# Kernel optimization log

Hardware: AMD Instinct MI355X
Metric: run time of the kernel (lower is better)

## Reference

```python
import jax, jax.numpy as jnp
import numpy as np
import itertools

R = 32  # voxel resolution
B, CIN, COUT, N, SD = 4, 32, 64, 32768, 256


def group_norm(x, gamma, beta, eps=1e-5):
    # torch GroupNorm with g = min(8, C) adjusted for divisibility
    C = x.shape[1]
    g = min(8, C)
    while g > 1 and C % g:
        g -= 1
    b = x.shape[0]
    xs = x.reshape(b, g, C // g, -1)
    mu = xs.mean(axis=(2, 3), keepdims=True)
    var = xs.var(axis=(2, 3), keepdims=True)
    xn = ((xs - mu) / jnp.sqrt(var + eps)).reshape(x.shape)
    shp = (1, C) + (1,) * (x.ndim - 2)
    return xn * gamma.reshape(shp) + beta.reshape(shp)


def conv1x1(w, x):  # w: (O, C), x: (B, C, N)
    return jnp.einsum('oc,bcn->bon', w, x)


def conv3d(x, w):  # x: (B,C,D,H,W), w: (O,I,3,3,3), padding 1
    return jax.lax.conv_general_dilated(x, w, (1, 1, 1), 'SAME',
                                        dimension_numbers=('NCDHW', 'OIDHW', 'NCDHW'))


def normalize_coords(coords):  # (B,N,3) -> [0, R-1]
    vmin = coords.min(axis=1, keepdims=True)
    vmax = coords.max(axis=1, keepdims=True)
    return (coords - vmin) / jnp.maximum(vmax - vmin, 1e-8) * (R - 1)


def voxelize(feats_bcn, norm):  # average voxelization via scatter-add
    b, C, n = feats_bcn.shape
    idx = jnp.clip(jnp.round(norm), 0, R - 1).astype(jnp.int32)  # (B,N,3)
    flat = (idx[..., 0] * R + idx[..., 1]) * R + idx[..., 2]  # (B,N)
    f_bnc = feats_bcn.transpose(0, 2, 1)
    seg = jax.vmap(lambda f, i: jax.ops.segment_sum(f, i, num_segments=R ** 3))(f_bnc, flat)
    cnt = jax.vmap(lambda i: jax.ops.segment_sum(jnp.ones((n,), feats_bcn.dtype), i, num_segments=R ** 3))(flat)
    vox = seg / jnp.maximum(cnt, 1.0)[..., None]  # (B, R^3, C)
    return vox.transpose(0, 2, 1).reshape(b, C, R, R, R)


def devoxelize(vox, norm):  # trilinear interpolation gather
    b, C = vox.shape[:2]
    n = norm.shape[1]
    f = jnp.clip(norm, 0.0, R - 1)
    x0 = jnp.floor(f)
    fr = f - x0
    x0i = x0.astype(jnp.int32)
    idxs, wts = [], []
    for d in itertools.product((0, 1), repeat=3):
        dv = jnp.array(d, jnp.int32)
        ci = jnp.minimum(x0i + dv, R - 1)  # (B,N,3)
        w = jnp.prod(jnp.where(jnp.array(d, bool), fr, 1.0 - fr), axis=-1)  # (B,N)
        idxs.append((ci[..., 0] * R + ci[..., 1]) * R + ci[..., 2])
        wts.append(w)
    idx8 = jnp.stack(idxs, axis=-1)  # (B,N,8)
    w8 = jnp.stack(wts, axis=-1)  # (B,N,8)
    vf = vox.reshape(b, C, R ** 3)
    g = jnp.take_along_axis(vf, idx8.reshape(b, 1, n * 8), axis=2).reshape(b, C, n, 8)
    return jnp.einsum('bcnk,bnk->bcn', g, w8)


def setup_inputs() -> dict:
    key = jax.random.key(0)
    ks = jax.random.split(key, 12)
    s = 0.05
    return {
        'feats': jax.random.normal(ks[0], (B, CIN, N), jnp.float32),
        'coords': jax.random.uniform(ks[1], (B, N, 3), jnp.float32),
        'style': jax.random.normal(ks[2], (B, SD), jnp.float32),
        'w_pin': jax.random.normal(ks[3], (COUT, CIN), jnp.float32) * s,
        'g_pin': jnp.ones((COUT,), jnp.float32), 'b_pin': jnp.zeros((COUT,), jnp.float32),
        'w_v1': jax.random.normal(ks[4], (COUT, COUT, 3, 3, 3), jnp.float32) * s,
        'g_v1': jnp.ones((COUT,), jnp.float32), 'b_v1': jnp.zeros((COUT,), jnp.float32),
        'w_v2': jax.random.normal(ks[5], (COUT, COUT, 3, 3, 3), jnp.float32) * s,
        'g_v2': jnp.ones((COUT,), jnp.float32), 'b_v2': jnp.zeros((COUT,), jnp.float32),
        'w_fuse': jax.random.normal(ks[6], (COUT, COUT), jnp.float32) * s,
        'g_f': jnp.ones((COUT,), jnp.float32), 'b_f': jnp.zeros((COUT,), jnp.float32),
        'w_skip': jax.random.normal(ks[7], (COUT, CIN), jnp.float32) * s,
        'w_as': jax.random.normal(ks[8], (COUT, SD), jnp.float32) * s,
        'b_as': jnp.zeros((COUT,), jnp.float32),
        'w_ab': jax.random.normal(ks[9], (COUT, SD), jnp.float32) * s,
        'b_ab': jnp.zeros((COUT,), jnp.float32),
    }


def reference(feats, coords, style, w_pin, g_pin, b_pin, w_v1, g_v1, b_v1,
              w_v2, g_v2, b_v2, w_fuse, g_f, b_f, w_skip, w_as, b_as, w_ab, b_ab):
    silu = jax.nn.silu
    x_in = silu(group_norm(conv1x1(w_pin, feats), g_pin, b_pin))  # point_in
    norm = normalize_coords(coords)
    vox = voxelize(x_in, norm)
    vox = silu(group_norm(conv3d(vox, w_v1), g_v1, b_v1))
    vox = silu(group_norm(conv3d(vox, w_v2), g_v2, b_v2))
    devox = devoxelize(vox, norm)
    out = silu(group_norm(conv1x1(w_fuse, devox), g_f, b_f))  # fuse
    out = out + conv1x1(w_skip, feats)  # skip (c_in != c_out)
    s = (style @ w_as.T + b_as)[..., None]  # AdaIN scale (B, C, 1)
    bb = (style @ w_ab.T + b_ab)[..., None]
    return out * (1.0 + s) + bb
```

## Files before the change

### kernel.cpp

```cpp
#include <hip/hip_runtime.h>
#include <hip/hip_bf16.h>
#include <math.h>

#define RR   32
#define RB   4
#define CIN  32
#define CO   64
#define NP   32768
#define SD   256
#define NVOX (RR*RR*RR)
#define GRP  8
#define CPG  8
#define GN_CNT 262144.0f
#define PR   34
#define PSLICE (PR*PR*CO)
#define PROW   (PR*CO)
#define PVOL   ((size_t)PR*PR*PR*CO)
#define WSL   73728

typedef __attribute__((ext_vector_type(8))) short short8;
typedef __attribute__((ext_vector_type(4))) float f32x4;
typedef __attribute__((ext_vector_type(16))) float f32x16;

__device__ inline float silu_f(float x){ return x / (1.f + __expf(-x)); }
__device__ inline float bf2f(ushort u){ uint v = ((uint)u)<<16; return *(float*)&v; }
__device__ inline ushort f2bf(float x){ __hip_bfloat16 h = __float2bfloat16(x); return *(ushort*)&h; }

__global__ void k_wpack(const float* __restrict__ w, short* __restrict__ wp){
    int i = blockIdx.x*256 + threadIdx.x;
    if (i >= 27*4*2*64) return;
    int l  = i & 63;
    int nt = (i>>6) & 1;
    int kc = (i>>7) & 3;
    int t  = i>>9;
    int oc = nt*32 + (l&31);
    int cib = kc*16 + (l>>5)*8;
    ushort out[8];
    #pragma unroll
    for (int j=0;j<8;j++) out[j] = f2bf(w[((oc*CO + cib + j))*27 + t]);
    *(uint4*)(wp + (size_t)i*8) = *(uint4*)out;
}

__global__ void k_adain(const float* __restrict__ style, const float* __restrict__ w_as,
                        const float* __restrict__ b_as, const float* __restrict__ w_ab,
                        const float* __restrict__ b_ab, float* __restrict__ sout,
                        float* __restrict__ bout){
    int t = threadIdx.x;
    int b = t >> 6, o = t & 63;
    const float* st = style + b*SD;
    float accs = b_as[o], accb = b_ab[o];
    for (int k=0;k<SD;k++){ float sv = st[k]; accs += sv*w_as[o*SD+k]; accb += sv*w_ab[o*SD+k]; }
    sout[t]=accs; bout[t]=accb;
}

__global__ void k_minmax(const float* __restrict__ coords, float* __restrict__ vmm){
    int b = blockIdx.x; int t = threadIdx.x;
    float mn[3]={1e30f,1e30f,1e30f}, mx[3]={-1e30f,-1e30f,-1e30f};
    const float* cp = coords + (size_t)b*NP*3;
    for (int n=t;n<NP;n+=256){
        #pragma unroll
        for(int d=0;d<3;d++){ float v = cp[n*3+d]; mn[d]=fminf(mn[d],v); mx[d]=fmaxf(mx[d],v);}
    }
    __shared__ float smn[256][3], smx[256][3];
    #pragma unroll
    for(int d=0;d<3;d++){ smn[t][d]=mn[d]; smx[t][d]=mx[d]; }
    __syncthreads();
    for(int s=128;s>0;s>>=1){
        if(t<s){
            #pragma unroll
            for(int d=0;d<3;d++){
                smn[t][d]=fminf(smn[t][d],smn[t+s][d]);
                smx[t][d]=fmaxf(smx[t][d],smx[t+s][d]);
            }
        }
        __syncthreads();
    }
    if(t<3){ vmm[b*6+t]=smn[0][t]; vmm[b*6+3+t]=smx[0][t]; }
}

__global__ __launch_bounds__(256) void k_pin(const float* __restrict__ feats, const float* __restrict__ w_pin,
                      ushort* __restrict__ ybuf, float* __restrict__ stats){
    __shared__ float sred[GRP*2];
    int t = threadIdx.x;
    if (t<GRP*2) sred[t]=0.f;
    __syncthreads();
    int l = t & 63, wv = t >> 6;
    int lc = l & 31, h = l >> 5;
    int p = blockIdx.x*128 + wv*32 + lc;
    int b = p >> 15, n = p & (NP-1);
    short8 aw[2][2];
    #pragma unroll
    for (int nt=0;nt<2;nt++)
    #pragma unroll
    for (int kc=0;kc<2;kc++){
        ushort tmp[8];
        #pragma unroll
        for (int j=0;j<8;j++) tmp[j]=f2bf(w_pin[(nt*32+lc)*CIN + kc*16 + h*8 + j]);
        aw[nt][kc]=*(short8*)tmp;
    }
    const float* fp = feats + (size_t)b*CIN*NP + n;
    short8 bf[2];
    #pragma unroll
    for (int kc=0;kc<2;kc++){
        ushort tmp[8];
        #pragma unroll
        for (int j=0;j<8;j++) tmp[j]=f2bf(fp[(size_t)(kc*16+h*8+j)*NP]);
        bf[kc]=*(short8*)tmp;
    }
    f32x16 acc0={}, acc1={};
    #pragma unroll
    for (int kc=0;kc<2;kc++){
        acc0 = __builtin_amdgcn_mfma_f32_32x32x16_bf16(aw[0][kc], bf[kc], acc0, 0,0,0);
        acc1 = __builtin_amdgcn_mfma_f32_32x32x16_bf16(aw[1][kc], bf[kc], acc1, 0,0,0);
    }
    ushort* yo = ybuf + (size_t)p*CO;
    float sg[8], qg[8];
    #pragma unroll
    for (int nt=0;nt<2;nt++){
        #pragma unroll
        for (int q=0;q<4;q++){
            ushort pk[4]; float s=0.f, qq=0.f;
            #pragma unroll
            for (int j=0;j<4;j++){
                float v = nt ? acc1[q*4+j] : acc0[q*4+j];
                pk[j]=f2bf(v); s+=v; qq+=v*v;
            }
            *(uint2*)(yo + nt*32 + q*8 + h*4) = *(uint2*)pk;
            sg[nt*4+q]=s; qg[nt*4+q]=qq;
        }
    }
    #pragma unroll
    for (int g=0;g<8;g++){
        float s=sg[g], q=qg[g];
        #pragma unroll
        for (int off=1; off<64; off<<=1){ s+=__shfl_xor(s,off); q+=__shfl_xor(q,off); }
        if (l==0){ atomicAdd(&sred[g*2],s); atomicAdd(&sred[g*2+1],q); }
    }
    __syncthreads();
    if (t<GRP){ atomicAdd(&stats[(b*GRP+t)*2], sred[t*2]); atomicAdd(&stats[(b*GRP+t)*2+1], sred[t*2+1]); }
}

__global__ __launch_bounds__(256) void k_count(const float* __restrict__ coords, const float* __restrict__ vmm,
                        int* __restrict__ pid, int* __restrict__ cnt){
    int p = blockIdx.x*256 + threadIdx.x;
    int b = p >> 15, n = p & (NP-1);
    const float* cp = coords + (size_t)(b*NP + n)*3;
    int id[3];
    #pragma unroll
    for(int d=0;d<3;d++){
        float vmin = vmm[b*6+d], vmax = vmm[b*6+3+d];
        float nr = (cp[d]-vmin)/fmaxf(vmax-vmin,1e-8f)*(RR-1);
        int ii = (int)rintf(nr);
        id[d] = min(max(ii,0),RR-1);
    }
    int flat = (id[0]*RR + id[1])*RR + id[2];
    pid[p] = flat;
    atomicAdd(&cnt[(b<<15)+flat], 1);
}

__global__ __launch_bounds__(1024) void k_scan(const int* __restrict__ cnt, int* __restrict__ offs,
                        int* __restrict__ cursor){
    int b = blockIdx.x, t = threadIdx.x;
    const int* c = cnt + (b<<15);
    int base = t*32;
    int pref[32];
    int s = 0;
    #pragma unroll
    for (int k4=0;k4<8;k4++){
        int4 q = *(const int4*)(c + base + k4*4);
        pref[k4*4+0]=s; s+=q.x;
        pref[k4*4+1]=s; s+=q.y;
        pref[k4*4+2]=s; s+=q.z;
        pref[k4*4+3]=s; s+=q.w;
    }
    int lane = t & 63, w = t >> 6;
    int inc = s;
    #pragma unroll
    for (int off=1; off<64; off<<=1){ int u = __shfl_up(inc, off); if (lane>=off) inc += u; }
    __shared__ int wsum[16];
    if (lane==63) wsum[w]=inc;
    __syncthreads();
    int wexcl=0;
    for (int i=0;i<w;i++) wexcl += wsum[i];
    int texcl = wexcl + inc - s;
    int* o = offs + (b<<15) + base;
    int* cu = cursor + (b<<15) + base;
    #pragma unroll
    for (int k=0;k<32;k++){ int v = texcl + pref[k]; o[k]=v; cu[k]=v; }
}

__global__ __launch_bounds__(256) void k_fill(const int* __restrict__ pid, int* __restrict__ cursor,
                       int* __restrict__ order){
    int p = blockIdx.x*256 + threadIdx.x;
    int b = p >> 15, n = p & (NP-1);
    int v = pid[p];
    int slot = atomicAdd(&cursor[(b<<15)+v], 1);
    order[(b<<15)+slot] = n;
}

__global__ __launch_bounds__(256) void k_gather_pad(const ushort* __restrict__ ybuf, const int* __restrict__ offs,
                             const int* __restrict__ order, const float* __restrict__ stats,
                             const float* __restrict__ gamma, const float* __restrict__ beta,
                             ushort* __restrict__ P){
    int i = blockIdx.x*256 + threadIdx.x;
    int c8 = i & 7;
    int vox = (i>>3) & (NVOX-1);
    int b = i >> 18;
    float s = stats[(b*GRP+c8)*2], qq = stats[(b*GRP+c8)*2+1];
    float m = s/GN_CNT;
    float inv = rsqrtf(qq/GN_CNT - m*m + 1e-5f);
    float ga[8], be[8];
    #pragma unroll
    for (int k=0;k<8;k++){ ga[k]=gamma[c8*8+k]*inv; be[k]=beta[c8*8+k]-m*ga[k]; }
    int o0 = offs[(b<<15)+vox];
    int o1 = (vox==NVOX-1) ? NP : offs[(b<<15)+vox+1];
    float acc[8];
    #pragma unroll
    for (int k=0;k<8;k++) acc[k]=0.f;
    for (int j=o0; j<o1; j++){
        int n = order[(b<<15)+j];
        uint4 raw = *(const uint4*)(ybuf + ((size_t)((b<<15)+n))*CO + c8*8);
        ushort* us = (ushort*)&raw;
        #pragma unroll
        for (int k=0;k<8;k++){
            float x = bf2f(us[k])*ga[k] + be[k];
            acc[k] += silu_f(x);
        }
    }
    float rc = (o1>o0) ? 1.f/(float)(o1-o0) : 0.f;
    ushort out[8];
    #pragma unroll
    for (int k=0;k<8;k++) out[k]=f2bf(acc[k]*rc);
    int u = vox>>10, v = (vox>>5)&31, w = vox&31;
    size_t pd = ((size_t)b*PVOL) + (size_t)(u+1)*PSLICE + (v+1)*PROW + (w+1)*CO + c8*8;
    *(uint4*)(P + pd) = *(uint4*)out;
}

__global__ __launch_bounds__(512, 2) void k_conv_mfma(const __hip_bfloat16* __restrict__ P,
                        const short* __restrict__ wpack,
                        __hip_bfloat16* __restrict__ outv, float* __restrict__ stats){
    __shared__ __align__(16) char lds[18*4352 + WSL];
    char* wlds = lds + 18*4352;
    int t = threadIdx.x;
    int blk = blockIdx.x;
    int vt = blk & 1;
    int u  = (blk >> 1) & 31;
    int b  = blk >> 6;
    int v0 = vt*16;

    const ushort* Pp = (const ushort*)P;
    int l  = t & 63;
    int wv = t >> 6;
    int lr = l & 31;
    int lh = l >> 5;

    f32x16 acc00 = {}, acc01 = {}, acc10 = {}, acc11 = {};

    for (int dz = 0; dz < 3; dz++){
        if (dz) __syncthreads();
        for (int i = t; i < 18*272; i += 512){
            int r = i / 272;
            int chunk = i - r*272;
            size_t src = (size_t)b*PVOL + (size_t)(u+dz)*PSLICE + (size_t)(v0+r)*PROW + (size_t)chunk*8;
            uint4 val = *(const uint4*)(Pp + src);
            int vx = chunk >> 3;
            int colb = (chunk & 7) << 4;
            int dst = r*4352 + vx*128 + (colb ^ ((vx&7)<<4));
            *(uint4*)(lds + dst) = val;
        }
        const uint4* wsrc = (const uint4*)(wpack + (size_t)dz*(WSL/2));
        uint4* wdst = (uint4*)wlds;
        for (int i = t; i < WSL/16; i += 512) wdst[i] = wsrc[i];
        __syncthreads();
        #pragma unroll
        for (int dy = 0; dy < 3; dy++){
            int ra_base = (2*wv + dy)*4352;
            #pragma unroll
            for (int dx = 0; dx < 3; dx++){
                int vx = lr + dx;
                int sw = (vx & 7) << 4;
                int abase = ra_base + vx*128;
                int wbase = ((dy*3 + dx)*4)*2048 + l*16;
                #pragma unroll
                for (int kc = 0; kc < 4; kc++){
                    short8 bw0 = *(const short8*)(wlds + wbase + kc*2048);
                    short8 bw1 = *(const short8*)(wlds + wbase + kc*2048 + 1024);
                    int col = (kc*32 + lh*16) ^ sw;
                    short8 av0 = *(const short8*)(lds + abase + col);
                    short8 av1 = *(const short8*)(lds + abase + 4352 + col);
                    acc00 = __builtin_amdgcn_mfma_f32_32x32x16_bf16(av0, bw0, acc00, 0, 0, 0);
                    acc01 = __builtin_amdgcn_mfma_f32_32x32x16_bf16(av0, bw1, acc01, 0, 0, 0);
                    acc10 = __builtin_amdgcn_mfma_f32_32x32x16_bf16(av1, bw0, acc10, 0, 0, 0);
                    acc11 = __builtin_amdgcn_mfma_f32_32x32x16_bf16(av1, bw1, acc11, 0, 0, 0);
                }
            }
        }
    }

    ushort* ob = (ushort*)outv;
    float s0 = 0.f, q0 = 0.f, s1 = 0.f, q1 = 0.f;
    size_t vrow0 = ((size_t)(b*32 + u)*32 + v0 + 2*wv);
    #pragma unroll
    for (int reg = 0; reg < 16; reg++){
        int x = (reg&3) + 8*(reg>>2) + 4*lh;
        float a, c;
        a = acc00[reg]; c = acc01[reg];
        s0 += a; q0 += a*a; s1 += c; q1 += c*c;
        ob[(vrow0*32 + x)*CO + lr]      = f2bf(a);
        ob[(vrow0*32 + x)*CO + 32 + lr] = f2bf(c);
        a = acc10[reg]; c = acc11[reg];
        s0 += a; q0 += a*a; s1 += c; q1 += c*c;
        ob[((vrow0+1)*32 + x)*CO + lr]      = f2bf(a);
        ob[((vrow0+1)*32 + x)*CO + 32 + lr] = f2bf(c);
    }
    #pragma unroll
    for (int off : {1,2,4,32}){
        s0 += __shfl_xor(s0, off); q0 += __shfl_xor(q0, off);
        s1 += __shfl_xor(s1, off); q1 += __shfl_xor(q1, off);
    }
    if (lh==0 && (lr&7)==0){
        int g0 = lr>>3;
        atomicAdd(&stats[(b*GRP+g0)*2],     s0);
        atomicAdd(&stats[(b*GRP+g0)*2+1],   q0);
        atomicAdd(&stats[(b*GRP+4+g0)*2],   s1);
        atomicAdd(&stats[(b*GRP+4+g0)*2+1], q1);
    }
}

__global__ __launch_bounds__(256) void k_gnfin_cast(const __hip_bfloat16* __restrict__ raw, const float* __restrict__ stats,
                        const float* __restrict__ gamma, const float* __restrict__ beta,
                        __hip_bfloat16* __restrict__ P){
    int i = blockIdx.x*256 + threadIdx.x;
    int c8 = i & 7;
    int vox = (i>>3) & (NVOX-1);
    int b = i >> 18;
    float s = stats[(b*GRP+c8)*2], qq = stats[(b*GRP+c8)*2+1];
    float m = s/GN_CNT;
    float inv = rsqrtf(qq/GN_CNT - m*m + 1e-5f);
    uint4 rv = *(const uint4*)((const ushort*)raw + ((size_t)i)*8);
    ushort* us = (ushort*)&rv;
    ushort out[8];
    #pragma unroll
    for (int j=0;j<8;j++){
        int c = c8*8+j;
        float x = (bf2f(us[j]) - m)*inv*gamma[c] + beta[c];
        out[j] = f2bf(silu_f(x));
    }
    int u = vox>>10, v = (vox>>5)&31, w = vox&31;
    size_t pd = ((size_t)b*PVOL) + (size_t)(u+1)*PSLICE + (v+1)*PROW + (w+1)*CO + c8*8;
    *(uint4*)((ushort*)P + pd) = *(uint4*)out;
}

__global__ __launch_bounds__(256) void k_gnfin_b16(__hip_bfloat16* __restrict__ raw, const float* __restrict__ stats,
                        const float* __restrict__ gamma, const float* __restrict__ beta){
    int i = blockIdx.x*256 + threadIdx.x;
    int c8 = i & 7;
    int b = i >> 18;
    float s = stats[(b*GRP+c8)*2], qq = stats[(b*GRP+c8)*2+1];
    float m = s/GN_CNT;
    float inv = rsqrtf(qq/GN_CNT - m*m + 1e-5f);
    uint4 rv = *(const uint4*)((const ushort*)raw + ((size_t)i)*8);
    ushort* us = (ushort*)&rv;
    ushort out[8];
    #pragma unroll
    for (int j=0;j<8;j++){
        int c = c8*8+j;
        float x = (bf2f(us[j]) - m)*inv*gamma[c] + beta[c];
        out[j] = f2bf(silu_f(x));
    }
    *(uint4*)((ushort*)raw + ((size_t)i)*8) = *(uint4*)out;
}

__global__ __launch_bounds__(256) void k_devox_fuse(const __hip_bfloat16* __restrict__ vox_, const float* __restrict__ coords,
                             const float* __restrict__ vmm, const float* __restrict__ wf,
                             ushort* __restrict__ obuf, float* __restrict__ stats){
    __shared__ float sred[GRP*2];
    int t = threadIdx.x;
    if (t<GRP*2) sred[t]=0.f;
    __syncthreads();
    int l = t & 63, wv = t >> 6;
    int lc = l & 31, h = l >> 5;
    int p = blockIdx.x*128 + wv*32 + lc;
    int b = p >> 15, n = p & (NP-1);
    short8 aw[2][4];
    #pragma unroll
    for (int nt=0;nt<2;nt++)
    #pragma unroll
    for (int kc=0;kc<4;kc++){
        ushort tmp[8];
        #pragma unroll
        for (int j=0;j<8;j++) tmp[j]=f2bf(wf[(nt*32+lc)*CO + kc*16 + h*8 + j]);
        aw[nt][kc]=*(short8*)tmp;
    }
    const float* cp = coords + (size_t)(b*NP+n)*3;
    float fr[3]; int x0[3];
    #pragma unroll
    for(int d=0;d<3;d++){
        float vmin=vmm[b*6+d], vmax=vmm[b*6+3+d];
        float nr = (cp[d]-vmin)/fmaxf(vmax-vmin,1e-8f)*(RR-1);
        nr = fminf(fmaxf(nr,0.f),(float)(RR-1));
        float fl = floorf(nr);
        x0[d]=(int)fl; fr[d]=nr-fl;
    }
    float dev[4][8] = {};
    const ushort* vb = (const ushort*)vox_ + (size_t)b*NVOX*CO;
    #pragma unroll
    for (int k=0;k<8;k++){
        int d0=(k>>2)&1, d1=(k>>1)&1, d2=k&1;
        int i0=min(x0[0]+d0,RR-1), i1=min(x0[1]+d1,RR-1), i2=min(x0[2]+d2,RR-1);
        float w = (d0?fr[0]:1.f-fr[0])*(d1?fr[1]:1.f-fr[1])*(d2?fr[2]:1.f-fr[2]);
        const ushort* vp = vb + (size_t)((i0*RR+i1)*RR+i2)*CO + h*8;
        #pragma unroll
        for (int kc=0;kc<4;kc++){
            uint4 rv = *(const uint4*)(vp + kc*16);
            ushort* us = (ushort*)&rv;
            #pragma unroll
            for (int j=0;j<8;j++) dev[kc][j] += w * bf2f(us[j]);
        }
    }
    short8 bf[4];
    #pragma unroll
    for (int kc=0;kc<4;kc++){
        ushort tmp[8];
        #pragma unroll
        for (int j=0;j<8;j++) tmp[j]=f2bf(dev[kc][j]);
        bf[kc]=*(short8*)tmp;
    }
    f32x16 acc0={}, acc1={};
    #pragma unroll
    for (int kc=0;kc<4;kc++){
        acc0 = __builtin_amdgcn_mfma_f32_32x32x16_bf16(aw[0][kc], bf[kc], acc0, 0,0,0);
        acc1 = __builtin_amdgcn_mfma_f32_32x32x16_bf16(aw[1][kc], bf[kc], acc1, 0,0,0);
    }
    ushort* op = obuf + (size_t)p*CO;
    float sg[8], qg[8];
    #pragma unroll
    for (int nt=0;nt<2;nt++){
        #pragma unroll
        for (int q=0;q<4;q++){
            ushort pk[4]; float s=0.f, qq=0.f;
            #pragma unroll
            for (int j=0;j<4;j++){
                float v = nt ? acc1[q*4+j] : acc0[q*4+j];
                pk[j]=f2bf(v); s+=v; qq+=v*v;
            }
            *(uint2*)(op + nt*32 + q*8 + h*4) = *(uint2*)pk;
            sg[nt*4+q]=s; qg[nt*4+q]=qq;
        }
    }
    #pragma unroll
    for (int g=0;g<8;g++){
        float s=sg[g], q=qg[g];
        #pragma unroll
        for (int off=1; off<64; off<<=1){ s+=__shfl_xor(s,off); q+=__shfl_xor(q,off); }
        if (l==0){ atomicAdd(&sred[g*2],s); atomicAdd(&sred[g*2+1],q); }
    }
    __syncthreads();
    if (t<GRP){ atomicAdd(&stats[(b*GRP+t)*2], sred[t*2]); atomicAdd(&stats[(b*GRP+t)*2+1], sred[t*2+1]); }
}

__global__ __launch_bounds__(256) void k_final(const ushort* __restrict__ obuf, const float* __restrict__ stats,
                        const float* __restrict__ gamma, const float* __restrict__ beta,
                        const float* __restrict__ feats, const float* __restrict__ wskip,
                        const float* __restrict__ ada_s, const float* __restrict__ ada_b,
                        float* __restrict__ out){
    int t = threadIdx.x;
    int l = t & 63, wv = t >> 6;
    int lc = l & 31, h = l >> 5;
    int p = blockIdx.x*128 + wv*32 + lc;
    int b = p >> 15, n = p & (NP-1);
    short8 aw[2][2];
    #pragma unroll
    for (int nt=0;nt<2;nt++)
    #pragma unroll
    for (int kc=0;kc<2;kc++){
        ushort tmp[8];
        #pragma unroll
        for (int j=0;j<8;j++) tmp[j]=f2bf(wskip[(nt*32+lc)*CIN + kc*16 + h*8 + j]);
        aw[nt][kc]=*(short8*)tmp;
    }
    const float* fp = feats + (size_t)b*CIN*NP + n;
    short8 bf[2];
    #pragma unroll
    for (int kc=0;kc<2;kc++){
        ushort tmp[8];
        #pragma unroll
        for (int j=0;j<8;j++) tmp[j]=f2bf(fp[(size_t)(kc*16+h*8+j)*NP]);
        bf[kc]=*(short8*)tmp;
    }
    f32x16 acc0={}, acc1={};
    #pragma unroll
    for (int kc=0;kc<2;kc++){
        acc0 = __builtin_amdgcn_mfma_f32_32x32x16_bf16(aw[0][kc], bf[kc], acc0, 0,0,0);
        acc1 = __builtin_amdgcn_mfma_f32_32x32x16_bf16(aw[1][kc], bf[kc], acc1, 0,0,0);
    }
    float mean[GRP], inv[GRP];
    #pragma unroll
    for (int g=0; g<GRP; g++){
        float s=stats[(b*GRP+g)*2], q=stats[(b*GRP+g)*2+1];
        float m=s/GN_CNT;
        mean[g]=m; inv[g]=rsqrtf(q/GN_CNT - m*m + 1e-5f);
    }
    const ushort* ip = obuf + (size_t)p*CO;
    float* op = out + (size_t)b*CO*NP + n;
    #pragma unroll
    for (int nt=0;nt<2;nt++){
        #pragma unroll
        for (int q=0;q<4;q++){
            uint2 raw = *(const uint2*)(ip + nt*32 + q*8 + h*4);
            ushort* us = (ushort*)&raw;
            int g = nt*4 + q;
            #pragma unroll
            for (int j=0;j<4;j++){
                int oc = nt*32 + q*8 + h*4 + j;
                float u = (bf2f(us[j]) - mean[g])*inv[g]*gamma[oc] + beta[oc];
                u = silu_f(u);
                float sk = nt ? acc1[q*4+j] : acc0[q*4+j];
                float s = ada_s[b*CO+oc], bb = ada_b[b*CO+oc];
                op[(size_t)oc*NP] = (u+sk)*(1.f+s)+bb;
            }
        }
    }
}

extern "C" void kernel_launch(void* const* d_in, const int* in_sizes, int n_in,
                              void* d_out, int out_size, void* d_ws, size_t ws_size,
                              hipStream_t stream){
    const float* feats =(const float*)d_in[0];
    const float* coords=(const float*)d_in[1];
    const float* style =(const float*)d_in[2];
    const float* w_pin =(const float*)d_in[3];
    const float* g_pin =(const float*)d_in[4];
    const float* b_pin =(const float*)d_in[5];
    const float* w_v1  =(const float*)d_in[6];
    const float* g_v1  =(const float*)d_in[7];
    const float* b_v1  =(const float*)d_in[8];
    const float* w_v2  =(const float*)d_in[9];
    const float* g_v2  =(const float*)d_in[10];
    const float* b_v2  =(const float*)d_in[11];
    const float* w_fuse=(const float*)d_in[12];
    const float* g_f   =(const float*)d_in[13];
    const float* b_f   =(const float*)d_in[14];
    const float* w_skip=(const float*)d_in[15];
    const float* w_as  =(const float*)d_in[16];
    const float* b_as  =(const float*)d_in[17];
    const float* w_ab  =(const float*)d_in[18];
    const float* b_ab  =(const float*)d_in[19];
    float* out=(float*)d_out;
    char* ws =(char*)d_ws;

    ushort* ybuf  = (ushort*)ws;
    ushort* Pvol  = (ushort*)(ws + 16777216);
    ushort* raw   = (ushort*)(ws + 16777216 + 20123648);
    char*   small = ws + 16777216 + 20123648 + 16777216;
    float* stats  = (float*)small;
    float* vmm    = stats + 256;
    float* ada_s  = vmm + 24;
    float* ada_b  = ada_s + RB*CO;
    short* wp1    = (short*)(ada_b + RB*CO);
    short* wp2    = wp1 + 27*4*2*64*8;
    int*   pid    = (int*)(wp2 + 27*4*2*64*8);
    int*   cnt    = pid + RB*NP;
    int*   offs   = cnt + RB*NVOX;
    int*   cursor = offs + RB*NVOX;
    int*   order  = cursor + RB*NVOX;
    ushort* obuf  = ybuf;

    float* st0 = stats;
    float* st1 = stats + 64;
    float* st2 = stats + 128;
    float* st3 = stats + 192;

    hipMemsetAsync(stats, 0, 256*sizeof(float), stream);
    hipMemsetAsync(cnt, 0, (size_t)RB*NVOX*sizeof(int), stream);
    hipMemsetAsync(Pvol, 0, (size_t)RB*PVOL*sizeof(ushort), stream);

    k_wpack<<<54,256,0,stream>>>(w_v1, wp1);
    k_wpack<<<54,256,0,stream>>>(w_v2, wp2);
    k_adain<<<1,256,0,stream>>>(style,w_as,b_as,w_ab,b_ab,ada_s,ada_b);
    k_minmax<<<RB,256,0,stream>>>(coords,vmm);

    k_pin<<<RB*NP/128,256,0,stream>>>(feats,w_pin,ybuf,st0);
    k_count<<<RB*NP/256,256,0,stream>>>(coords,vmm,pid,cnt);
    k_scan<<<RB,1024,0,stream>>>(cnt,offs,cursor);
    k_fill<<<RB*NP/256,256,0,stream>>>(pid,cursor,order);
    k_gather_pad<<<RB*NVOX*8/256,256,0,stream>>>(ybuf,offs,order,st0,g_pin,b_pin,Pvol);

    k_conv_mfma<<<RB*RR*2,512,0,stream>>>((const __hip_bfloat16*)Pvol, wp1, (__hip_bfloat16*)raw, st1);
    k_gnfin_cast<<<RB*NVOX*8/256,256,0,stream>>>((const __hip_bfloat16*)raw, st1, g_v1, b_v1, (__hip_bfloat16*)Pvol);
    k_conv_mfma<<<RB*RR*2,512,0,stream>>>((const __hip_bfloat16*)Pvol, wp2, (__hip_bfloat16*)raw, st2);
    k_gnfin_b16<<<RB*NVOX*8/256,256,0,stream>>>((__hip_bfloat16*)raw, st2, g_v2, b_v2);

    k_devox_fuse<<<RB*NP/128,256,0,stream>>>((const __hip_bfloat16*)raw, coords, vmm, w_fuse, obuf, st3);
    k_final<<<RB*NP/128,256,0,stream>>>(obuf, st3, g_f, b_f, feats, w_skip, ada_s, ada_b, out);
}
```

Baseline: 422.7 us.

## Merge prep kernels, scatter point features in voxel order, retile 3D conv

Folds weight packing, AdaIN projection, stats zeroing and coordinate min/max into one prep launch. The counting sort now runs before the point-in conv, so k_pin writes each point's features straight to its sorted slot and gather_pad reads contiguously instead of going through an order indirection. The 3D conv block shrinks from 512 to 256 threads covering 8 rows instead of 16, with per-dy weight slices staged in smaller LDS, giving more blocks and less LDS per block. The cost is more barriers per block and more halo reloads of the input slab across blocks.

```diff
diff --git a/kernel.cpp b/kernel.cpp
--- a/kernel.cpp
+++ b/kernel.cpp
@@ -16,7 +16,6 @@
 #define PSLICE (PR*PR*CO)
 #define PROW   (PR*CO)
 #define PVOL   ((size_t)PR*PR*PR*CO)
-#define WSL   73728
 
 typedef __attribute__((ext_vector_type(8))) short short8;
 typedef __attribute__((ext_vector_type(4))) float f32x4;
@@ -26,9 +25,7 @@
 __device__ inline float bf2f(ushort u){ uint v = ((uint)u)<<16; return *(float*)&v; }
 __device__ inline ushort f2bf(float x){ __hip_bfloat16 h = __float2bfloat16(x); return *(ushort*)&h; }
 
-__global__ void k_wpack(const float* __restrict__ w, short* __restrict__ wp){
-    int i = blockIdx.x*256 + threadIdx.x;
-    if (i >= 27*4*2*64) return;
+__device__ inline void wpack_dev(const float* __restrict__ w, short* __restrict__ wp, int i){
     int l  = i & 63;
     int nt = (i>>6) & 1;
     int kc = (i>>7) & 3;
@@ -41,44 +38,113 @@
     *(uint4*)(wp + (size_t)i*8) = *(uint4*)out;
 }
 
-__global__ void k_adain(const float* __restrict__ style, const float* __restrict__ w_as,
-                        const float* __restrict__ b_as, const float* __restrict__ w_ab,
-                        const float* __restrict__ b_ab, float* __restrict__ sout,
-                        float* __restrict__ bout){
-    int t = threadIdx.x;
-    int b = t >> 6, o = t & 63;
-    const float* st = style + b*SD;
-    float accs = b_as[o], accb = b_ab[o];
-    for (int k=0;k<SD;k++){ float sv = st[k]; accs += sv*w_as[o*SD+k]; accb += sv*w_ab[o*SD+k]; }
-    sout[t]=accs; bout[t]=accb;
-}
-
-__global__ void k_minmax(const float* __restrict__ coords, float* __restrict__ vmm){
-    int b = blockIdx.x; int t = threadIdx.x;
-    float mn[3]={1e30f,1e30f,1e30f}, mx[3]={-1e30f,-1e30f,-1e30f};
-    const float* cp = coords + (size_t)b*NP*3;
-    for (int n=t;n<NP;n+=256){
-        #pragma unroll
-        for(int d=0;d<3;d++){ float v = cp[n*3+d]; mn[d]=fminf(mn[d],v); mx[d]=fmaxf(mx[d],v);}
-    }
+__global__ __launch_bounds__(256) void k_prep(const float* __restrict__ w_v1, const float* __restrict__ w_v2,
+                      short* __restrict__ wp1, short* __restrict__ wp2,
+                      const float* __restrict__ style, const float* __restrict__ w_as,
+                      const float* __restrict__ b_as, const float* __restrict__ w_ab,
+                      const float* __restrict__ b_ab, float* __restrict__ ada_s,
+                      float* __restrict__ ada_b, float* __restrict__ stats,
+                      const float* __restrict__ coords, float* __restrict__ vmm){
     __shared__ float smn[256][3], smx[256][3];
-    #pragma unroll
-    for(int d=0;d<3;d++){ smn[t][d]=mn[d]; smx[t][d]=mx[d]; }
+    int blk = blockIdx.x, t = threadIdx.x;
+    if (blk < 54){
+        int i = blk*256 + t;
+        if (i < 27*4*2*64) wpack_dev(w_v1, wp1, i);
+    } else if (blk < 108){
+        int i = (blk-54)*256 + t;
+        if (i < 27*4*2*64) wpack_dev(w_v2, wp2, i);
+    } else if (blk == 108){
+        stats[t] = 0.f;
+        int b = t >> 6, o = t & 63;
+        const float* st = style + b*SD;
+        float accs = b_as[o], accb = b_ab[o];
+        for (int k=0;k<SD;k++){ float sv = st[k]; accs += sv*w_as[o*SD+k]; accb += sv*w_ab[o*SD+k]; }
+        ada_s[t]=accs; ada_b[t]=accb;
+    } else {
+        int b = blk - 109;
+        float mn[3]={1e30f,1e30f,1e30f}, mx[3]={-1e30f,-1e30f,-1e30f};
+        const float* cp = coords + (size_t)b*NP*3;
+        for (int n=t;n<NP;n+=256){
+            #pragma unroll
+            for(int d=0;d<3;d++){ float v = cp[n*3+d]; mn[d]=fminf(mn[d],v); mx[d]=fmaxf(mx[d],v);}
+        }
+        #pragma unroll
+        for(int d=0;d<3;d++){ smn[t][d]=mn[d]; smx[t][d]=mx[d]; }
+        __syncthreads();
+        for(int s=128;s>0;s>>=1){
+            if(t<s){
+                #pragma unroll
+                for(int d=0;d<3;d++){
+                    smn[t][d]=fminf(smn[t][d],smn[t+s][d]);
+                    smx[t][d]=fmaxf(smx[t][d],smx[t+s][d]);
+                }
+            }
+            __syncthreads();
+        }
+        if(t<3){ vmm[b*6+t]=smn[0][t]; vmm[b*6+3+t]=smx[0][t]; }
+    }
+}
+
+__global__ __launch_bounds__(256) void k_count(const float* __restrict__ coords, const float* __restrict__ vmm,
+                        int* __restrict__ pid, int* __restrict__ cnt){
+    int p = blockIdx.x*256 + threadIdx.x;
+    int b = p >> 15, n = p & (NP-1);
+    const float* cp = coords + (size_t)(b*NP + n)*3;
+    int id[3];
+    #pragma unroll
+    for(int d=0;d<3;d++){
+        float vmin = vmm[b*6+d], vmax = vmm[b*6+3+d];
+        float nr = (cp[d]-vmin)/fmaxf(vmax-vmin,1e-8f)*(RR-1);
+        int ii = (int)rintf(nr);
+        id[d] = min(max(ii,0),RR-1);
+    }
+    int flat = (id[0]*RR + id[1])*RR + id[2];
+    pid[p] = flat;
+    atomicAdd(&cnt[(b<<15)+flat], 1);
+}
+
+__global__ __launch_bounds__(1024) void k_scan(const int* __restrict__ cnt, int* __restrict__ offs,
+                        int* __restrict__ cursor){
+    int b = blockIdx.x, t = threadIdx.x;
+    const int* c = cnt + (b<<15);
+    int base = t*32;
+    int pref[32];
+    int s = 0;
+    #pragma unroll
+    for (int k4=0;k4<8;k4++){
+        int4 q = *(const int4*)(c + base + k4*4);
+        pref[k4*4+0]=s; s+=q.x;
+        pref[k4*4+1]=s; s+=q.y;
+        pref[k4*4+2]=s; s+=q.z;
+        pref[k4*4+3]=s; s+=q.w;
+    }
+    int lane = t & 63, w = t >> 6;
+    int inc = s;
+    #pragma unroll
+    for (int off=1; off<64; off<<=1){ int u = __shfl_up(inc, off); if (lane>=off) inc += u; }
+    __shared__ int wsum[16];
+    if (lane==63) wsum[w]=inc;
     __syncthreads();
-    for(int s=128;s>0;s>>=1){
-        if(t<s){
-            #pragma unroll
-            for(int d=0;d<3;d++){
-                smn[t][d]=fminf(smn[t][d],smn[t+s][d]);
-                smx[t][d]=fmaxf(smx[t][d],smx[t+s][d]);
-            }
-        }
-        __syncthreads();
-    }
-    if(t<3){ vmm[b*6+t]=smn[0][t]; vmm[b*6+3+t]=smx[0][t]; }
+    int wexcl=0;
+    for (int i=0;i<w;i++) wexcl += wsum[i];
+    int texcl = wexcl + inc - s;
+    int* o = offs + (b<<15) + base;
+    int* cu = cursor + (b<<15) + base;
+    #pragma unroll
+    for (int k=0;k<32;k++){ int v = texcl + pref[k]; o[k]=v; cu[k]=v; }
+}
+
+__global__ __launch_bounds__(256) void k_fill(const int* __restrict__ pid, int* __restrict__ cursor,
+                       int* __restrict__ slotmap){
+    int p = blockIdx.x*256 + threadIdx.x;
+    int b = p >> 15;
+    int v = pid[p];
+    int slot = atomicAdd(&cursor[(b<<15)+v], 1);
+    slotmap[p] = slot;
 }
 
 __global__ __launch_bounds__(256) void k_pin(const float* __restrict__ feats, const float* __restrict__ w_pin,
+                      const int* __restrict__ slotmap,
                       ushort* __restrict__ ybuf, float* __restrict__ stats){
     __shared__ float sred[GRP*2];
     int t = threadIdx.x;
@@ -113,7 +179,8 @@
         acc0 = __builtin_amdgcn_mfma_f32_32x32x16_bf16(aw[0][kc], bf[kc], acc0, 0,0,0);
         acc1 = __builtin_amdgcn_mfma_f32_32x32x16_bf16(aw[1][kc], bf[kc], acc1, 0,0,0);
     }
-    ushort* yo = ybuf + (size_t)p*CO;
+    int slot = slotmap[p];
+    ushort* yo = ybuf + ((size_t)(b<<15) + slot)*CO;
     float sg[8], qg[8];
     #pragma unroll
     for (int nt=0;nt<2;nt++){
@@ -140,66 +207,8 @@
     if (t<GRP){ atomicAdd(&stats[(b*GRP+t)*2], sred[t*2]); atomicAdd(&stats[(b*GRP+t)*2+1], sred[t*2+1]); }
 }
 
-__global__ __launch_bounds__(256) void k_count(const float* __restrict__ coords, const float* __restrict__ vmm,
-                        int* __restrict__ pid, int* __restrict__ cnt){
-    int p = blockIdx.x*256 + threadIdx.x;
-    int b = p >> 15, n = p & (NP-1);
-    const float* cp = coords + (size_t)(b*NP + n)*3;
-    int id[3];
-    #pragma unroll
-    for(int d=0;d<3;d++){
-        float vmin = vmm[b*6+d], vmax = vmm[b*6+3+d];
-        float nr = (cp[d]-vmin)/fmaxf(vmax-vmin,1e-8f)*(RR-1);
-        int ii = (int)rintf(nr);
-        id[d] = min(max(ii,0),RR-1);
-    }
-    int flat = (id[0]*RR + id[1])*RR + id[2];
-    pid[p] = flat;
-    atomicAdd(&cnt[(b<<15)+flat], 1);
-}
-
-__global__ __launch_bounds__(1024) void k_scan(const int* __restrict__ cnt, int* __restrict__ offs,
-                        int* __restrict__ cursor){
-    int b = blockIdx.x, t = threadIdx.x;
-    const int* c = cnt + (b<<15);
-    int base = t*32;
-    int pref[32];
-    int s = 0;
-    #pragma unroll
-    for (int k4=0;k4<8;k4++){
-        int4 q = *(const int4*)(c + base + k4*4);
-        pref[k4*4+0]=s; s+=q.x;
-        pref[k4*4+1]=s; s+=q.y;
-        pref[k4*4+2]=s; s+=q.z;
-        pref[k4*4+3]=s; s+=q.w;
-    }
-    int lane = t & 63, w = t >> 6;
-    int inc = s;
-    #pragma unroll
-    for (int off=1; off<64; off<<=1){ int u = __shfl_up(inc, off); if (lane>=off) inc += u; }
-    __shared__ int wsum[16];
-    if (lane==63) wsum[w]=inc;
-    __syncthreads();
-    int wexcl=0;
-    for (int i=0;i<w;i++) wexcl += wsum[i];
-    int texcl = wexcl + inc - s;
-    int* o = offs + (b<<15) + base;
-    int* cu = cursor + (b<<15) + base;
-    #pragma unroll
-    for (int k=0;k<32;k++){ int v = texcl + pref[k]; o[k]=v; cu[k]=v; }
-}
-
-__global__ __launch_bounds__(256) void k_fill(const int* __restrict__ pid, int* __restrict__ cursor,
-                       int* __restrict__ order){
-    int p = blockIdx.x*256 + threadIdx.x;
-    int b = p >> 15, n = p & (NP-1);
-    int v = pid[p];
-    int slot = atomicAdd(&cursor[(b<<15)+v], 1);
-    order[(b<<15)+slot] = n;
-}
-
 __global__ __launch_bounds__(256) void k_gather_pad(const ushort* __restrict__ ybuf, const int* __restrict__ offs,
-                             const int* __restrict__ order, const float* __restrict__ stats,
+                             const float* __restrict__ stats,
                              const float* __restrict__ gamma, const float* __restrict__ beta,
                              ushort* __restrict__ P){
     int i = blockIdx.x*256 + threadIdx.x;
@@ -218,8 +227,7 @@
     #pragma unroll
     for (int k=0;k<8;k++) acc[k]=0.f;
     for (int j=o0; j<o1; j++){
-        int n = order[(b<<15)+j];
-        uint4 raw = *(const uint4*)(ybuf + ((size_t)((b<<15)+n))*CO + c8*8);
+        uint4 raw = *(const uint4*)(ybuf + ((size_t)((b<<15)+j))*CO + c8*8);
         ushort* us = (ushort*)&raw;
         #pragma unroll
         for (int k=0;k<8;k++){
@@ -236,17 +244,17 @@
     *(uint4*)(P + pd) = *(uint4*)out;
 }
 
-__global__ __launch_bounds__(512, 2) void k_conv_mfma(const __hip_bfloat16* __restrict__ P,
+__global__ __launch_bounds__(256, 2) void k_conv_mfma(const __hip_bfloat16* __restrict__ P,
                         const short* __restrict__ wpack,
                         __hip_bfloat16* __restrict__ outv, float* __restrict__ stats){
-    __shared__ __align__(16) char lds[18*4352 + WSL];
-    char* wlds = lds + 18*4352;
+    __shared__ __align__(16) char lds[10*4352 + 24576];
+    char* wlds = lds + 10*4352;
     int t = threadIdx.x;
     int blk = blockIdx.x;
-    int vt = blk & 1;
-    int u  = (blk >> 1) & 31;
-    int b  = blk >> 6;
-    int v0 = vt*16;
+    int vt = blk & 3;
+    int u  = (blk >> 2) & 31;
+    int b  = blk >> 7;
+    int v0 = vt*8;
 
     const ushort* Pp = (const ushort*)P;
     int l  = t & 63;
@@ -257,43 +265,41 @@
     f32x16 acc00 = {}, acc01 = {}, acc10 = {}, acc11 = {};
 
     for (int dz = 0; dz < 3; dz++){
-        if (dz) __syncthreads();
-        for (int i = t; i < 18*272; i += 512){
+        for (int i = t; i < 2720; i += 256){
             int r = i / 272;
             int chunk = i - r*272;
             size_t src = (size_t)b*PVOL + (size_t)(u+dz)*PSLICE + (size_t)(v0+r)*PROW + (size_t)chunk*8;
             uint4 val = *(const uint4*)(Pp + src);
             int vx = chunk >> 3;
             int colb = (chunk & 7) << 4;
-            int dst = r*4352 + vx*128 + (colb ^ ((vx&7)<<4));
-            *(uint4*)(lds + dst) = val;
-        }
-        const uint4* wsrc = (const uint4*)(wpack + (size_t)dz*(WSL/2));
-        uint4* wdst = (uint4*)wlds;
-        for (int i = t; i < WSL/16; i += 512) wdst[i] = wsrc[i];
-        __syncthreads();
-        #pragma unroll
+            *(uint4*)(lds + r*4352 + vx*128 + (colb ^ ((vx&7)<<4))) = val;
+        }
         for (int dy = 0; dy < 3; dy++){
-            int ra_base = (2*wv + dy)*4352;
+            const uint4* wsrc = (const uint4*)(wpack + (size_t)(dz*9 + dy*3)*4096);
+            uint4* wdst = (uint4*)wlds;
+            #pragma unroll
+            for (int i=0;i<6;i++) wdst[t + i*256] = wsrc[t + i*256];
+            __syncthreads();
             #pragma unroll
             for (int dx = 0; dx < 3; dx++){
                 int vx = lr + dx;
                 int sw = (vx & 7) << 4;
-                int abase = ra_base + vx*128;
-                int wbase = ((dy*3 + dx)*4)*2048 + l*16;
+                int ra = (2*wv + dy)*4352 + vx*128;
+                int wb = dx*8192 + l*16;
                 #pragma unroll
                 for (int kc = 0; kc < 4; kc++){
-                    short8 bw0 = *(const short8*)(wlds + wbase + kc*2048);
-                    short8 bw1 = *(const short8*)(wlds + wbase + kc*2048 + 1024);
+                    short8 bw0 = *(const short8*)(wlds + wb + kc*2048);
+                    short8 bw1 = *(const short8*)(wlds + wb + kc*2048 + 1024);
                     int col = (kc*32 + lh*16) ^ sw;
-                    short8 av0 = *(const short8*)(lds + abase + col);
-                    short8 av1 = *(const short8*)(lds + abase + 4352 + col);
+                    short8 av0 = *(const short8*)(lds + ra + col);
+                    short8 av1 = *(const short8*)(lds + ra + 4352 + col);
                     acc00 = __builtin_amdgcn_mfma_f32_32x32x16_bf16(av0, bw0, acc00, 0, 0, 0);
                     acc01 = __builtin_amdgcn_mfma_f32_32x32x16_bf16(av0, bw1, acc01, 0, 0, 0);
                     acc10 = __builtin_amdgcn_mfma_f32_32x32x16_bf16(av1, bw0, acc10, 0, 0, 0);
                     acc11 = __builtin_amdgcn_mfma_f32_32x32x16_bf16(av1, bw1, acc11, 0, 0, 0);
                 }
             }
+            __syncthreads();
         }
     }
 
@@ -563,7 +569,7 @@
     int*   cnt    = pid + RB*NP;
     int*   offs   = cnt + RB*NVOX;
     int*   cursor = offs + RB*NVOX;
-    int*   order  = cursor + RB*NVOX;
+    int*   slotmap= cursor + RB*NVOX;
     ushort* obuf  = ybuf;
 
     float* st0 = stats;
@@ -571,24 +577,20 @@
     float* st2 = stats + 128;
     float* st3 = stats + 192;
 
-    hipMemsetAsync(stats, 0, 256*sizeof(float), stream);
     hipMemsetAsync(cnt, 0, (size_t)RB*NVOX*sizeof(int), stream);
     hipMemsetAsync(Pvol, 0, (size_t)RB*PVOL*sizeof(ushort), stream);
 
-    k_wpack<<<54,256,0,stream>>>(w_v1, wp1);
-    k_wpack<<<54,256,0,stream>>>(w_v2, wp2);
-    k_adain<<<1,256,0,stream>>>(style,w_as,b_as,w_ab,b_ab,ada_s,ada_b);
-    k_minmax<<<RB,256,0,stream>>>(coords,vmm);
-
-    k_pin<<<RB*NP/128,256,0,stream>>>(feats,w_pin,ybuf,st0);
+    k_prep<<<113,256,0,stream>>>(w_v1,w_v2,wp1,wp2,style,w_as,b_as,w_ab,b_ab,
+                                 ada_s,ada_b,stats,coords,vmm);
     k_count<<<RB*NP/256,256,0,stream>>>(coords,vmm,pid,cnt);
     k_scan<<<RB,1024,0,stream>>>(cnt,offs,cursor);
-    k_fill<<<RB*NP/256,256,0,stream>>>(pid,cursor,order);
-    k_gather_pad<<<RB*NVOX*8/256,256,0,stream>>>(ybuf,offs,order,st0,g_pin,b_pin,Pvol);
-
-    k_conv_mfma<<<RB*RR*2,512,0,stream>>>((const __hip_bfloat16*)Pvol, wp1, (__hip_bfloat16*)raw, st1);
+    k_fill<<<RB*NP/256,256,0,stream>>>(pid,cursor,slotmap);
+    k_pin<<<RB*NP/128,256,0,stream>>>(feats,w_pin,slotmap,ybuf,st0);
+    k_gather_pad<<<RB*NVOX*8/256,256,0,stream>>>(ybuf,offs,st0,g_pin,b_pin,Pvol);
+
+    k_conv_mfma<<<RB*RR*4,256,0,stream>>>((const __hip_bfloat16*)Pvol, wp1, (__hip_bfloat16*)raw, st1);
     k_gnfin_cast<<<RB*NVOX*8/256,256,0,stream>>>((const __hip_bfloat16*)raw, st1, g_v1, b_v1, (__hip_bfloat16*)Pvol);
-    k_conv_mfma<<<RB*RR*2,512,0,stream>>>((const __hip_bfloat16*)Pvol, wp2, (__hip_bfloat16*)raw, st2);
+    k_conv_mfma<<<RB*RR*4,256,0,stream>>>((const __hip_bfloat16*)Pvol, wp2, (__hip_bfloat16*)raw, st2);
     k_gnfin_b16<<<RB*NVOX*8/256,256,0,stream>>>((__hip_bfloat16*)raw, st2, g_v2, b_v2);
 
     k_devox_fuse<<<RB*NP/128,256,0,stream>>>((const __hip_bfloat16*)raw, coords, vmm, w_fuse, obuf, st3);
```

Result: faster. 387.4 us (-8.4%).
